# Performance work log

Measured on AMD Instinct MI355X. Metric: run time of the kernel, lower is better.

The kernel has to match this reference:

```python
import jax, jax.numpy as jnp
import numpy as np

B, T, D, H = 131072, 30, 10, 20
EPS = 1e-5


def setup_inputs() -> dict:
    key = jax.random.key(0)
    ks = jax.random.split(key, 8)
    rn = lambda k, s: (jax.random.normal(k, s, dtype=jnp.float32) * 0.1)
    return {
        "x": jax.random.normal(ks[0], (B, T, D), dtype=jnp.float32),
        "g0": jnp.ones((T, 2 * D), jnp.float32),
        "be0": jnp.zeros((T, 2 * D), jnp.float32),
        "W1": rn(ks[1], (T, H, 2 * D)),
        "b1": rn(ks[2], (T, H)),
        "g1": jnp.ones((T, H), jnp.float32),
        "be1": jnp.zeros((T, H), jnp.float32),
        "W2": rn(ks[3], (T, H, H)),
        "b2": rn(ks[4], (T, H)),
        "g2": jnp.ones((T, H), jnp.float32),
        "be2": jnp.zeros((T, H), jnp.float32),
        "W3": rn(ks[5], (T, D, H)),
        "b3": rn(ks[6], (T, D)),
    }


def _bn(x, g, b):
    # training-mode BatchNorm1d: batch stats, biased variance, eps=1e-5
    mu = x.mean(0)
    var = ((x - mu) ** 2).mean(0)
    return (x - mu) * jax.lax.rsqrt(var + EPS) * g + b


def _forward(x, g0, be0, W1, b1, g1, be1, W2, b2, g2, be2, W3, b3):
    xs = jnp.swapaxes(x, 0, 1)  # [T, B, D] time-major

    def step(prev, ps):
        xt, g0t, be0t, W1t, b1t, g1t, be1t, W2t, b2t, g2t, be2t, W3t, b3t = ps
        h = jnp.concatenate([xt, prev], axis=1)      # [B, 2D] recurrent concat
        h = _bn(h, g0t, be0t)
        h = jax.nn.relu(_bn(h @ W1t.T + b1t, g1t, be1t))  # [B, H]
        h = jax.nn.relu(_bn(h @ W2t.T + b2t, g2t, be2t))  # [B, H]
        out = h @ W3t.T + b3t                              # [B, D]
        return out, out

    init = jnp.zeros((x.shape[0], D), dtype=x.dtype)
    _, outs = jax.lax.scan(step, init, (xs, g0, be0, W1, b1, g1, be1, W2, b2, g2, be2, W3, b3))
    return jnp.swapaxes(outs, 0, 1)  # [B, T, D]


def reference(x, g0, be0, W1, b1, g1, be1, W2, b2, g2, be2, W3, b3):
    return _forward(x, g0, be0, W1, b1, g1, be1, W2, b2, g2, be2, W3, b3)
```

## Files before the change

kernel.cpp:

```cpp
#include <hip/hip_runtime.h>

static constexpr int   BATCH = 131072;
static constexpr int   TS    = 30;
static constexpr int   DD    = 10;
static constexpr int   HH    = 20;
static constexpr float EPSV  = 1e-5f;
static constexpr float INV_B = 1.0f / (float)BATCH;

static constexpr int NBLK = 256;
static constexpr int NTHR = 256;
static constexpr int RPT  = 2;
static constexpr int TT   = NBLK * NTHR;
static constexpr int NS   = 8;
static constexpr int GRPS = 8;
static constexpr int GSZ  = NBLK / GRPS;
static constexpr int NVA  = 230;
static constexpr int NVB  = 40;
static constexpr int STRA = NVA * NS;
static constexpr int STRB = NVB * NS;
static constexpr int CTRW = 160;
static constexpr int NPH  = 2 * TS + 1;

__device__ __forceinline__ int tri(int k, int l) {
    return k * (41 - k) / 2 + (l - k);
}

template <int CTRL>
__device__ __forceinline__ float dpp_add(float v) {
    int x = __builtin_amdgcn_update_dpp(0, __float_as_int(v), CTRL, 0xF, 0xF, true);
    return v + __int_as_float(x);
}

__device__ __forceinline__ float rowsum16(float v) {
    v = dpp_add<0x111>(v);
    v = dpp_add<0x112>(v);
    v = dpp_add<0x114>(v);
    v = dpp_add<0x118>(v);
    return v;
}

__device__ __forceinline__ float aloadf(const float* p) {
    return __hip_atomic_load(p, __ATOMIC_RELAXED, __HIP_MEMORY_SCOPE_AGENT);
}

__device__ __forceinline__ void gbar(unsigned* __restrict__ base, int tid, int grp8) {
    __syncthreads();
    if (tid == 0) {
        if (__hip_atomic_fetch_add(base + grp8 * 16, 1u, __ATOMIC_RELAXED,
                                   __HIP_MEMORY_SCOPE_AGENT) == (unsigned)(GSZ - 1))
            __hip_atomic_fetch_add(base + 128, 1u, __ATOMIC_RELAXED,
                                   __HIP_MEMORY_SCOPE_AGENT);
        while (__hip_atomic_load(base + 128, __ATOMIC_RELAXED,
                                 __HIP_MEMORY_SCOPE_AGENT) < (unsigned)GRPS)
            __builtin_amdgcn_s_sleep(1);
    }
    __syncthreads();
}

__global__ void __launch_bounds__(NTHR)
rnn_all(const float* __restrict__ x, float* __restrict__ outg,
        const float* __restrict__ W1, const float* __restrict__ W2,
        const float* __restrict__ W3, const float* __restrict__ b3,
        const float* __restrict__ g0, const float* __restrict__ be0,
        const float* __restrict__ g1, const float* __restrict__ be1,
        const float* __restrict__ g2, const float* __restrict__ be2,
        float* __restrict__ redA, float* __restrict__ redB,
        unsigned* __restrict__ ctr)
{
    __shared__ float lred[16 * NVA];
    __shared__ float sM[230], sMu[20], sCov[400], sU[400], sP[400];
    __shared__ float sW1[400], sW2[400], sW3[200], sB3[10];
    __shared__ float sA0[20], sC0[20], sA1[20], sC1[20], sA2[20], sC2[20];

    const int tid     = threadIdx.x;
    const int grp     = tid >> 4;
    const bool lane15 = (tid & 15) == 15;
    const int slot    = blockIdx.x & (NS - 1);
    const int grp8    = blockIdx.x & (GRPS - 1);
    const int gt      = blockIdx.x * NTHR + tid;

    float pv[RPT][DD];
#pragma unroll
    for (int r = 0; r < RPT; ++r)
#pragma unroll
        for (int d = 0; d < DD; ++d) pv[r][d] = 0.0f;

    float xv[RPT][DD];
#pragma unroll
    for (int r = 0; r < RPT; ++r) {
        const float2* px = reinterpret_cast<const float2*>(x + (size_t)(gt + r * TT) * TS * DD);
#pragma unroll
        for (int i = 0; i < 5; ++i) { float2 v = px[i]; xv[r][2 * i] = v.x; xv[r][2 * i + 1] = v.y; }
    }

#define H0A(i) ((i) < DD ? xv[0][i] : 0.0f)
#define H0B(i) ((i) < DD ? xv[1][i] : 0.0f)
    {
        int v = 0;
#pragma unroll
        for (int k = 0; k < 2 * DD; ++k) {
#pragma unroll
            for (int l = k; l < 2 * DD; ++l) {
                float p = fmaf(H0A(k), H0A(l), H0B(k) * H0B(l));
                float r = rowsum16(p);
                if (lane15) lred[grp * NVA + v] = r;
                ++v;
            }
        }
#pragma unroll
        for (int k = 0; k < 2 * DD; ++k) {
            float r = rowsum16(H0A(k) + H0B(k));
            if (lane15) lred[grp * NVA + 210 + k] = r;
        }
    }
#undef H0A
#undef H0B
    __syncthreads();
    if (tid < NVA) {
        float acc = 0.0f;
#pragma unroll
        for (int g = 0; g < 16; ++g) acc += lred[g * NVA + tid];
        atomicAdd(redA + tid * NS + slot, acc);
    }
    gbar(ctr + (size_t)(2 * TS) * CTRW, tid, grp8);

    for (int t = 0; t < TS; ++t) {
        for (int i = tid; i < 400; i += NTHR) { sW1[i] = W1[t * 400 + i]; sW2[i] = W2[t * 400 + i]; }
        if (tid < 200) sW3[tid] = W3[t * 200 + tid];
        if (tid >= 200 && tid < 210) sB3[tid - 200] = b3[t * DD + (tid - 200)];

        float xn[RPT][DD];
        if (t + 1 < TS) {
#pragma unroll
            for (int r = 0; r < RPT; ++r) {
                const float2* px = reinterpret_cast<const float2*>(x + (size_t)(gt + r * TT) * TS * DD + (t + 1) * DD);
#pragma unroll
                for (int i = 0; i < 5; ++i) { float2 v = px[i]; xn[r][2 * i] = v.x; xn[r][2 * i + 1] = v.y; }
            }
        }

        if (tid < NVA) {
            const float* p = redA + (size_t)t * STRA + tid * NS;
            float s = 0.0f;
#pragma unroll
            for (int i = 0; i < NS; ++i) s += aloadf(p + i);
            sM[tid] = s;
        }
        __syncthreads();

        if (tid < 20) {
            float mu  = sM[210 + tid] * INV_B;
            float var = fmaf(-mu, mu, sM[tri(tid, tid)] * INV_B);
            float a   = g0[t * 20 + tid] * rsqrtf(var + EPSV);
            sA0[tid] = a;
            sC0[tid] = fmaf(-mu, a, be0[t * 20 + tid]);
            sMu[tid] = mu;
        }
        __syncthreads();

        for (int i = tid; i < 400; i += NTHR) {
            int k = i / 20, l = i % 20;
            int a = k < l ? k : l, b = k < l ? l : k;
            sCov[i] = fmaf(-sMu[k], sMu[l], sM[tri(a, b)] * INV_B);
            sU[i]   = sW1[i] * sA0[l];
        }
        __syncthreads();

        for (int i = tid; i < 400; i += NTHR) {
            int j = i / 20, k = i % 20;
            float acc = 0.0f;
#pragma unroll
            for (int l = 0; l < 20; ++l)
                acc = fmaf(sCov[k * 20 + l], sU[j * 20 + l], acc);
            sP[i] = acc * sU[i];
        }
        __syncthreads();

        if (tid < 20) {
            float var1 = 0.0f, m1 = 0.0f;
#pragma unroll
            for (int k = 0; k < 20; ++k) {
                var1 += sP[tid * 20 + k];
                m1    = fmaf(sU[tid * 20 + k], sMu[k], m1);
                m1    = fmaf(sW1[tid * 20 + k], sC0[k], m1);
            }
            float a1 = g1[t * 20 + tid] * rsqrtf(var1 + EPSV);
            sA1[tid] = a1;
            sC1[tid] = fmaf(-m1, a1, be1[t * 20 + tid]);
        }
        __syncthreads();

        float y2[RPT][HH];
#pragma unroll
        for (int r = 0; r < RPT; ++r) {
            float hn[20];
#pragma unroll
            for (int k = 0; k < 10; ++k) hn[k]      = fmaf(xv[r][k], sA0[k],      sC0[k]);
#pragma unroll
            for (int k = 0; k < 10; ++k) hn[10 + k] = fmaf(pv[r][k], sA0[10 + k], sC0[10 + k]);

            float h1[20];
#pragma unroll
            for (int j = 0; j < 20; ++j) {
                float y = 0.0f;
#pragma unroll
                for (int k = 0; k < 20; ++k) y = fmaf(sW1[j * 20 + k], hn[k], y);
                h1[j] = fmaxf(fmaf(y, sA1[j], sC1[j]), 0.0f);
            }
#pragma unroll
            for (int j = 0; j < 20; ++j) {
                float y = 0.0f;
#pragma unroll
                for (int k = 0; k < 20; ++k) y = fmaf(sW2[j * 20 + k], h1[k], y);
                y2[r][j] = y;
            }
        }

#pragma unroll
        for (int j = 0; j < 20; ++j) {
            float r = rowsum16(y2[0][j] + y2[1][j]);
            if (lane15) lred[grp * NVA + j] = r;
        }
#pragma unroll
        for (int j = 0; j < 20; ++j) {
            float r = rowsum16(fmaf(y2[0][j], y2[0][j], y2[1][j] * y2[1][j]));
            if (lane15) lred[grp * NVA + 20 + j] = r;
        }
        __syncthreads();
        if (tid < NVB) {
            float acc = 0.0f;
#pragma unroll
            for (int g = 0; g < 16; ++g) acc += lred[g * NVA + tid];
            atomicAdd(redB + (size_t)t * STRB + tid * NS + slot, acc);
        }

        gbar(ctr + (size_t)(2 * t) * CTRW, tid, grp8);

        if (tid < NVB) {
            const float* p = redB + (size_t)t * STRB + tid * NS;
            float s = 0.0f;
#pragma unroll
            for (int i = 0; i < NS; ++i) s += aloadf(p + i);
            sM[tid] = s;
        }
        __syncthreads();
        if (tid < 20) {
            float m   = sM[tid] * INV_B;
            float var = fmaf(-m, m, sM[20 + tid] * INV_B);
            float a   = g2[t * 20 + tid] * rsqrtf(var + EPSV);
            sA2[tid] = a;
            sC2[tid] = fmaf(-m, a, be2[t * 20 + tid]);
        }
        __syncthreads();

        float ov[RPT][DD];
#pragma unroll
        for (int r = 0; r < RPT; ++r) {
            float h2[20];
#pragma unroll
            for (int j = 0; j < 20; ++j)
                h2[j] = fmaxf(fmaf(y2[r][j], sA2[j], sC2[j]), 0.0f);
#pragma unroll
            for (int d = 0; d < DD; ++d) {
                float a = sB3[d];
#pragma unroll
                for (int j = 0; j < 20; ++j)
                    a = fmaf(sW3[d * 20 + j], h2[j], a);
                ov[r][d] = a;
            }
            float2* po = reinterpret_cast<float2*>(outg + (size_t)(gt + r * TT) * TS * DD + t * DD);
#pragma unroll
            for (int i = 0; i < 5; ++i) po[i] = make_float2(ov[r][2 * i], ov[r][2 * i + 1]);
#pragma unroll
            for (int d = 0; d < DD; ++d) pv[r][d] = ov[r][d];
        }

        if (t + 1 < TS) {
#define H0A(i) ((i) < DD ? xn[0][i] : ov[0][(i) - DD])
#define H0B(i) ((i) < DD ? xn[1][i] : ov[1][(i) - DD])
            {
                int v = 0;
#pragma unroll
                for (int k = 0; k < 2 * DD; ++k) {
#pragma unroll
                    for (int l = k; l < 2 * DD; ++l) {
                        float p = fmaf(H0A(k), H0A(l), H0B(k) * H0B(l));
                        float r = rowsum16(p);
                        if (lane15) lred[grp * NVA + v] = r;
                        ++v;
                    }
                }
#pragma unroll
                for (int k = 0; k < 2 * DD; ++k) {
                    float r = rowsum16(H0A(k) + H0B(k));
                    if (lane15) lred[grp * NVA + 210 + k] = r;
                }
            }
#undef H0A
#undef H0B
            __syncthreads();
            if (tid < NVA) {
                float acc = 0.0f;
#pragma unroll
                for (int g = 0; g < 16; ++g) acc += lred[g * NVA + tid];
                atomicAdd(redA + (size_t)(t + 1) * STRA + tid * NS + slot, acc);
            }
            gbar(ctr + (size_t)(2 * t + 1) * CTRW, tid, grp8);

#pragma unroll
            for (int r = 0; r < RPT; ++r)
#pragma unroll
                for (int d = 0; d < DD; ++d) xv[r][d] = xn[r][d];
        }
    }
}

extern "C" void kernel_launch(void* const* d_in, const int* in_sizes, int n_in,
                              void* d_out, int out_size, void* d_ws, size_t ws_size,
                              hipStream_t stream) {
    const float* x   = (const float*)d_in[0];
    const float* g0  = (const float*)d_in[1];
    const float* be0 = (const float*)d_in[2];
    const float* W1  = (const float*)d_in[3];
    const float* b1  = (const float*)d_in[4];   (void)b1;
    const float* g1  = (const float*)d_in[5];
    const float* be1 = (const float*)d_in[6];
    const float* W2  = (const float*)d_in[7];
    const float* b2  = (const float*)d_in[8];   (void)b2;
    const float* g2  = (const float*)d_in[9];
    const float* be2 = (const float*)d_in[10];
    const float* W3  = (const float*)d_in[11];
    const float* b3  = (const float*)d_in[12];
    float* out = (float*)d_out;

    const size_t redA_f = (size_t)TS * STRA;
    const size_t redB_f = (size_t)TS * STRB;
    const size_t ctr_u  = (size_t)NPH * CTRW;
    float*    redA  = (float*)d_ws;
    float*    redB  = redA + redA_f;
    unsigned* ctr   = (unsigned*)(redB + redB_f);

    hipMemsetAsync(d_ws, 0, (redA_f + redB_f) * 4 + ctr_u * 4, stream);

    rnn_all<<<NBLK, NTHR, 0, stream>>>(x, out, W1, W2, W3, b3,
                                       g0, be0, g1, be1, g2, be2,
                                       redA, redB, ctr);
}
```

Before: 1.299 ms.

## Process one row per thread with 512 blocks and two blocks per CU

Switches from two batch rows per thread over 256 blocks to one row per thread over 512 blocks, with launch bounds requesting two resident blocks per CU. The grid barrier is widened to 16 groups with a larger counter stride. The aim is more resident waves and more latency hiding, in exchange for twice as many blocks taking part in each grid barrier and in the atomic reductions. It also loses the per-thread amortisation of the DPP row reductions across two rows.

```diff
diff --git a/kernel.cpp b/kernel.cpp
--- a/kernel.cpp
+++ b/kernel.cpp
@@ -7,18 +7,16 @@
 static constexpr float EPSV  = 1e-5f;
 static constexpr float INV_B = 1.0f / (float)BATCH;
 
-static constexpr int NBLK = 256;
+static constexpr int NBLK = 512;
 static constexpr int NTHR = 256;
-static constexpr int RPT  = 2;
-static constexpr int TT   = NBLK * NTHR;
 static constexpr int NS   = 8;
-static constexpr int GRPS = 8;
+static constexpr int GRPS = 16;
 static constexpr int GSZ  = NBLK / GRPS;
 static constexpr int NVA  = 230;
 static constexpr int NVB  = 40;
 static constexpr int STRA = NVA * NS;
 static constexpr int STRB = NVB * NS;
-static constexpr int CTRW = 160;
+static constexpr int CTRW = 288;
 static constexpr int NPH  = 2 * TS + 1;
 
 __device__ __forceinline__ int tri(int k, int l) {
@@ -43,21 +41,21 @@
     return __hip_atomic_load(p, __ATOMIC_RELAXED, __HIP_MEMORY_SCOPE_AGENT);
 }
 
-__device__ __forceinline__ void gbar(unsigned* __restrict__ base, int tid, int grp8) {
+__device__ __forceinline__ void gbar(unsigned* __restrict__ base, int tid, int grpN) {
     __syncthreads();
     if (tid == 0) {
-        if (__hip_atomic_fetch_add(base + grp8 * 16, 1u, __ATOMIC_RELAXED,
+        if (__hip_atomic_fetch_add(base + grpN * 16, 1u, __ATOMIC_RELAXED,
                                    __HIP_MEMORY_SCOPE_AGENT) == (unsigned)(GSZ - 1))
-            __hip_atomic_fetch_add(base + 128, 1u, __ATOMIC_RELAXED,
+            __hip_atomic_fetch_add(base + 256, 1u, __ATOMIC_RELAXED,
                                    __HIP_MEMORY_SCOPE_AGENT);
-        while (__hip_atomic_load(base + 128, __ATOMIC_RELAXED,
+        while (__hip_atomic_load(base + 256, __ATOMIC_RELAXED,
                                  __HIP_MEMORY_SCOPE_AGENT) < (unsigned)GRPS)
             __builtin_amdgcn_s_sleep(1);
     }
     __syncthreads();
 }
 
-__global__ void __launch_bounds__(NTHR)
+__global__ void __launch_bounds__(NTHR, 2)
 rnn_all(const float* __restrict__ x, float* __restrict__ outg,
         const float* __restrict__ W1, const float* __restrict__ W2,
         const float* __restrict__ W3, const float* __restrict__ b3,
@@ -76,45 +74,39 @@
     const int grp     = tid >> 4;
     const bool lane15 = (tid & 15) == 15;
     const int slot    = blockIdx.x & (NS - 1);
-    const int grp8    = blockIdx.x & (GRPS - 1);
-    const int gt      = blockIdx.x * NTHR + tid;
-
-    float pv[RPT][DD];
-#pragma unroll
-    for (int r = 0; r < RPT; ++r)
-#pragma unroll
-        for (int d = 0; d < DD; ++d) pv[r][d] = 0.0f;
-
-    float xv[RPT][DD];
-#pragma unroll
-    for (int r = 0; r < RPT; ++r) {
-        const float2* px = reinterpret_cast<const float2*>(x + (size_t)(gt + r * TT) * TS * DD);
-#pragma unroll
-        for (int i = 0; i < 5; ++i) { float2 v = px[i]; xv[r][2 * i] = v.x; xv[r][2 * i + 1] = v.y; }
-    }
-
-#define H0A(i) ((i) < DD ? xv[0][i] : 0.0f)
-#define H0B(i) ((i) < DD ? xv[1][i] : 0.0f)
+    const int grpN    = blockIdx.x & (GRPS - 1);
+    const int row     = blockIdx.x * NTHR + tid;
+
+    float pv[DD];
+#pragma unroll
+    for (int d = 0; d < DD; ++d) pv[d] = 0.0f;
+
+    float xv[DD];
+    {
+        const float2* px = reinterpret_cast<const float2*>(x + (size_t)row * TS * DD);
+#pragma unroll
+        for (int i = 0; i < 5; ++i) { float2 v = px[i]; xv[2 * i] = v.x; xv[2 * i + 1] = v.y; }
+    }
+
+#define H0(i) ((i) < DD ? xv[i] : 0.0f)
     {
         int v = 0;
 #pragma unroll
         for (int k = 0; k < 2 * DD; ++k) {
 #pragma unroll
             for (int l = k; l < 2 * DD; ++l) {
-                float p = fmaf(H0A(k), H0A(l), H0B(k) * H0B(l));
-                float r = rowsum16(p);
+                float r = rowsum16(H0(k) * H0(l));
                 if (lane15) lred[grp * NVA + v] = r;
                 ++v;
             }
         }
 #pragma unroll
         for (int k = 0; k < 2 * DD; ++k) {
-            float r = rowsum16(H0A(k) + H0B(k));
+            float r = rowsum16(H0(k));
             if (lane15) lred[grp * NVA + 210 + k] = r;
         }
     }
-#undef H0A
-#undef H0B
+#undef H0
     __syncthreads();
     if (tid < NVA) {
         float acc = 0.0f;
@@ -122,21 +114,18 @@
         for (int g = 0; g < 16; ++g) acc += lred[g * NVA + tid];
         atomicAdd(redA + tid * NS + slot, acc);
     }
-    gbar(ctr + (size_t)(2 * TS) * CTRW, tid, grp8);
+    gbar(ctr + (size_t)(2 * TS) * CTRW, tid, grpN);
 
     for (int t = 0; t < TS; ++t) {
         for (int i = tid; i < 400; i += NTHR) { sW1[i] = W1[t * 400 + i]; sW2[i] = W2[t * 400 + i]; }
         if (tid < 200) sW3[tid] = W3[t * 200 + tid];
         if (tid >= 200 && tid < 210) sB3[tid - 200] = b3[t * DD + (tid - 200)];
 
-        float xn[RPT][DD];
+        float xn[DD];
         if (t + 1 < TS) {
-#pragma unroll
-            for (int r = 0; r < RPT; ++r) {
-                const float2* px = reinterpret_cast<const float2*>(x + (size_t)(gt + r * TT) * TS * DD + (t + 1) * DD);
-#pragma unroll
-                for (int i = 0; i < 5; ++i) { float2 v = px[i]; xn[r][2 * i] = v.x; xn[r][2 * i + 1] = v.y; }
-            }
+            const float2* px = reinterpret_cast<const float2*>(x + (size_t)row * TS * DD + (t + 1) * DD);
+#pragma unroll
+            for (int i = 0; i < 5; ++i) { float2 v = px[i]; xn[2 * i] = v.x; xn[2 * i + 1] = v.y; }
         }
 
         if (tid < NVA) {
@@ -190,14 +179,13 @@
         }
         __syncthreads();
 
-        float y2[RPT][HH];
-#pragma unroll
-        for (int r = 0; r < RPT; ++r) {
+        float y2[HH];
+        {
             float hn[20];
 #pragma unroll
-            for (int k = 0; k < 10; ++k) hn[k]      = fmaf(xv[r][k], sA0[k],      sC0[k]);
-#pragma unroll
-            for (int k = 0; k < 10; ++k) hn[10 + k] = fmaf(pv[r][k], sA0[10 + k], sC0[10 + k]);
+            for (int k = 0; k < 10; ++k) hn[k]      = fmaf(xv[k], sA0[k],      sC0[k]);
+#pragma unroll
+            for (int k = 0; k < 10; ++k) hn[10 + k] = fmaf(pv[k], sA0[10 + k], sC0[10 + k]);
 
             float h1[20];
 #pragma unroll
@@ -212,18 +200,18 @@
                 float y = 0.0f;
 #pragma unroll
                 for (int k = 0; k < 20; ++k) y = fmaf(sW2[j * 20 + k], h1[k], y);
-                y2[r][j] = y;
+                y2[j] = y;
             }
         }
 
 #pragma unroll
         for (int j = 0; j < 20; ++j) {
-            float r = rowsum16(y2[0][j] + y2[1][j]);
+            float r = rowsum16(y2[j]);
             if (lane15) lred[grp * NVA + j] = r;
         }
 #pragma unroll
         for (int j = 0; j < 20; ++j) {
-            float r = rowsum16(fmaf(y2[0][j], y2[0][j], y2[1][j] * y2[1][j]));
+            float r = rowsum16(y2[j] * y2[j]);
             if (lane15) lred[grp * NVA + 20 + j] = r;
         }
         __syncthreads();
@@ -234,7 +222,7 @@
             atomicAdd(redB + (size_t)t * STRB + tid * NS + slot, acc);
         }
 
-        gbar(ctr + (size_t)(2 * t) * CTRW, tid, grp8);
+        gbar(ctr + (size_t)(2 * t) * CTRW, tid, grpN);
 
         if (tid < NVB) {
             const float* p = redB + (size_t)t * STRB + tid * NS;
@@ -253,51 +241,47 @@
         }
         __syncthreads();
 
-        float ov[RPT][DD];
-#pragma unroll
-        for (int r = 0; r < RPT; ++r) {
+        float ov[DD];
+        {
             float h2[20];
 #pragma unroll
             for (int j = 0; j < 20; ++j)
-                h2[j] = fmaxf(fmaf(y2[r][j], sA2[j], sC2[j]), 0.0f);
+                h2[j] = fmaxf(fmaf(y2[j], sA2[j], sC2[j]), 0.0f);
 #pragma unroll
             for (int d = 0; d < DD; ++d) {
                 float a = sB3[d];
 #pragma unroll
                 for (int j = 0; j < 20; ++j)
                     a = fmaf(sW3[d * 20 + j], h2[j], a);
-                ov[r][d] = a;
-            }
-            float2* po = reinterpret_cast<float2*>(outg + (size_t)(gt + r * TT) * TS * DD + t * DD);
-#pragma unroll
-            for (int i = 0; i < 5; ++i) po[i] = make_float2(ov[r][2 * i], ov[r][2 * i + 1]);
-#pragma unroll
-            for (int d = 0; d < DD; ++d) pv[r][d] = ov[r][d];
+                ov[d] = a;
+            }
+            float2* po = reinterpret_cast<float2*>(outg + (size_t)row * TS * DD + t * DD);
+#pragma unroll
+            for (int i = 0; i < 5; ++i) po[i] = make_float2(ov[2 * i], ov[2 * i + 1]);
+#pragma unroll
+            for (int d = 0; d < DD; ++d) pv[d] = ov[d];
         }
 
         if (t + 1 < TS) {
-#define H0A(i) ((i) < DD ? xn[0][i] : ov[0][(i) - DD])
-#define H0B(i) ((i) < DD ? xn[1][i] : ov[1][(i) - DD])
+#define H0(i) ((i) < DD ? xn[i] : ov[(i) - DD])
             {
                 int v = 0;
 #pragma unroll
                 for (int k = 0; k < 2 * DD; ++k) {
 #pragma unroll
                     for (int l = k; l < 2 * DD; ++l) {
-                        float p = fmaf(H0A(k), H0A(l), H0B(k) * H0B(l));
-                        float r = rowsum16(p);
+                        float r = rowsum16(H0(k) * H0(l));
                         if (lane15) lred[grp * NVA + v] = r;
                         ++v;
                     }
                 }
 #pragma unroll
                 for (int k = 0; k < 2 * DD; ++k) {
-                    float r = rowsum16(H0A(k) + H0B(k));
+                    float r = rowsum16(H0(k));
                     if (lane15) lred[grp * NVA + 210 + k] = r;
                 }
             }
-#undef H0A
-#undef H0B
+#undef H0
             __syncthreads();
             if (tid < NVA) {
                 float acc = 0.0f;
@@ -305,12 +289,10 @@
                 for (int g = 0; g < 16; ++g) acc += lred[g * NVA + tid];
                 atomicAdd(redA + (size_t)(t + 1) * STRA + tid * NS + slot, acc);
             }
-            gbar(ctr + (size_t)(2 * t + 1) * CTRW, tid, grp8);
-
-#pragma unroll
-            for (int r = 0; r < RPT; ++r)
-#pragma unroll
-                for (int d = 0; d < DD; ++d) xv[r][d] = xn[r][d];
+            gbar(ctr + (size_t)(2 * t + 1) * CTRW, tid, grpN);
+
+#pragma unroll
+            for (int d = 0; d < DD; ++d) xv[d] = xn[d];
         }
     }
 }
```

After: 3.671 ms. 2.82x slower.

## Precompute x-only covariance terms before barrier and widen barrier groups to 16

Applied to the files above, without the earlier changes.

The layer-0 BatchNorm statistics for the next step are split: the x-only second moments and sums (which depend only on the prefetched next input) are now reduced and atomically accumulated before the mid-step grid barrier, leaving only the x·prev cross terms and prev-only terms on the critical path after the output is known. The hierarchical grid barrier also uses 16 groups instead of 8, with the counter stride widened to fit. This shortens the serialized work between the last two barriers of each step, at the cost of an extra block-level sync and more atomics earlier in the step.

```diff
diff --git a/kernel.cpp b/kernel.cpp
--- a/kernel.cpp
+++ b/kernel.cpp
@@ -12,13 +12,13 @@
 static constexpr int RPT  = 2;
 static constexpr int TT   = NBLK * NTHR;
 static constexpr int NS   = 8;
-static constexpr int GRPS = 8;
+static constexpr int GRPS = 16;
 static constexpr int GSZ  = NBLK / GRPS;
 static constexpr int NVA  = 230;
 static constexpr int NVB  = 40;
 static constexpr int STRA = NVA * NS;
 static constexpr int STRB = NVB * NS;
-static constexpr int CTRW = 160;
+static constexpr int CTRW = 272;
 static constexpr int NPH  = 2 * TS + 1;
 
 __device__ __forceinline__ int tri(int k, int l) {
@@ -43,14 +43,14 @@
     return __hip_atomic_load(p, __ATOMIC_RELAXED, __HIP_MEMORY_SCOPE_AGENT);
 }
 
-__device__ __forceinline__ void gbar(unsigned* __restrict__ base, int tid, int grp8) {
+__device__ __forceinline__ void gbar(unsigned* __restrict__ base, int tid, int grpN) {
     __syncthreads();
     if (tid == 0) {
-        if (__hip_atomic_fetch_add(base + grp8 * 16, 1u, __ATOMIC_RELAXED,
+        if (__hip_atomic_fetch_add(base + grpN * 16, 1u, __ATOMIC_RELAXED,
                                    __HIP_MEMORY_SCOPE_AGENT) == (unsigned)(GSZ - 1))
-            __hip_atomic_fetch_add(base + 128, 1u, __ATOMIC_RELAXED,
+            __hip_atomic_fetch_add(base + 256, 1u, __ATOMIC_RELAXED,
                                    __HIP_MEMORY_SCOPE_AGENT);
-        while (__hip_atomic_load(base + 128, __ATOMIC_RELAXED,
+        while (__hip_atomic_load(base + 256, __ATOMIC_RELAXED,
                                  __HIP_MEMORY_SCOPE_AGENT) < (unsigned)GRPS)
             __builtin_amdgcn_s_sleep(1);
     }
@@ -76,7 +76,7 @@
     const int grp     = tid >> 4;
     const bool lane15 = (tid & 15) == 15;
     const int slot    = blockIdx.x & (NS - 1);
-    const int grp8    = blockIdx.x & (GRPS - 1);
+    const int grpN    = blockIdx.x & (GRPS - 1);
     const int gt      = blockIdx.x * NTHR + tid;
 
     float pv[RPT][DD];
@@ -122,7 +122,7 @@
         for (int g = 0; g < 16; ++g) acc += lred[g * NVA + tid];
         atomicAdd(redA + tid * NS + slot, acc);
     }
-    gbar(ctr + (size_t)(2 * TS) * CTRW, tid, grp8);
+    gbar(ctr + (size_t)(2 * TS) * CTRW, tid, grpN);
 
     for (int t = 0; t < TS; ++t) {
         for (int i = tid; i < 400; i += NTHR) { sW1[i] = W1[t * 400 + i]; sW2[i] = W2[t * 400 + i]; }
@@ -198,7 +198,6 @@
             for (int k = 0; k < 10; ++k) hn[k]      = fmaf(xv[r][k], sA0[k],      sC0[k]);
 #pragma unroll
             for (int k = 0; k < 10; ++k) hn[10 + k] = fmaf(pv[r][k], sA0[10 + k], sC0[10 + k]);
-
             float h1[20];
 #pragma unroll
             for (int j = 0; j < 20; ++j) {
@@ -214,6 +213,41 @@
                 for (int k = 0; k < 20; ++k) y = fmaf(sW2[j * 20 + k], h1[k], y);
                 y2[r][j] = y;
             }
+        }
+
+        if (t + 1 < TS) {
+            int c = 0;
+#pragma unroll
+            for (int k = 0; k < DD; ++k) {
+#pragma unroll
+                for (int l = k; l < DD; ++l) {
+                    float p = fmaf(xn[0][k], xn[0][l], xn[1][k] * xn[1][l]);
+                    float r = rowsum16(p);
+                    if (lane15) lred[grp * NVA + c] = r;
+                    ++c;
+                }
+            }
+#pragma unroll
+            for (int k = 0; k < DD; ++k) {
+                float r = rowsum16(xn[0][k] + xn[1][k]);
+                if (lane15) lred[grp * NVA + 55 + k] = r;
+            }
+            __syncthreads();
+            if (tid < 65) {
+                float acc = 0.0f;
+#pragma unroll
+                for (int g = 0; g < 16; ++g) acc += lred[g * NVA + tid];
+                int v;
+                if (tid < 55) {
+                    int c2 = tid, k = 0;
+                    while (c2 >= DD - k) { c2 -= DD - k; ++k; }
+                    v = tri(k, k + c2);
+                } else {
+                    v = 210 + (tid - 55);
+                }
+                atomicAdd(redA + (size_t)(t + 1) * STRA + v * NS + slot, acc);
+            }
+            __syncthreads();
         }
 
 #pragma unroll
@@ -234,7 +268,7 @@
             atomicAdd(redB + (size_t)t * STRB + tid * NS + slot, acc);
         }
 
-        gbar(ctr + (size_t)(2 * t) * CTRW, tid, grp8);
+        gbar(ctr + (size_t)(2 * t) * CTRW, tid, grpN);
 
         if (tid < NVB) {
             const float* p = redB + (size_t)t * STRB + tid * NS;
@@ -276,36 +310,52 @@
         }
 
         if (t + 1 < TS) {
-#define H0A(i) ((i) < DD ? xn[0][i] : ov[0][(i) - DD])
-#define H0B(i) ((i) < DD ? xn[1][i] : ov[1][(i) - DD])
             {
-                int v = 0;
-#pragma unroll
-                for (int k = 0; k < 2 * DD; ++k) {
-#pragma unroll
-                    for (int l = k; l < 2 * DD; ++l) {
-                        float p = fmaf(H0A(k), H0A(l), H0B(k) * H0B(l));
+                int c = 0;
+#pragma unroll
+                for (int k = 0; k < DD; ++k) {
+#pragma unroll
+                    for (int l = 0; l < DD; ++l) {
+                        float p = fmaf(xn[0][k], ov[0][l], xn[1][k] * ov[1][l]);
                         float r = rowsum16(p);
-                        if (lane15) lred[grp * NVA + v] = r;
-                        ++v;
+                        if (lane15) lred[grp * NVA + c] = r;
+                        ++c;
                     }
                 }
 #pragma unroll
-                for (int k = 0; k < 2 * DD; ++k) {
-                    float r = rowsum16(H0A(k) + H0B(k));
-                    if (lane15) lred[grp * NVA + 210 + k] = r;
-                }
-            }
-#undef H0A
-#undef H0B
+                for (int a = 0; a < DD; ++a) {
+#pragma unroll
+                    for (int b = a; b < DD; ++b) {
+                        float p = fmaf(ov[0][a], ov[0][b], ov[1][a] * ov[1][b]);
+                        float r = rowsum16(p);
+                        if (lane15) lred[grp * NVA + c] = r;
+                        ++c;
+                    }
+                }
+#pragma unroll
+                for (int d = 0; d < DD; ++d) {
+                    float r = rowsum16(ov[0][d] + ov[1][d]);
+                    if (lane15) lred[grp * NVA + 155 + d] = r;
+                }
+            }
             __syncthreads();
-            if (tid < NVA) {
+            if (tid < 165) {
                 float acc = 0.0f;
 #pragma unroll
                 for (int g = 0; g < 16; ++g) acc += lred[g * NVA + tid];
-                atomicAdd(redA + (size_t)(t + 1) * STRA + tid * NS + slot, acc);
-            }
-            gbar(ctr + (size_t)(2 * t + 1) * CTRW, tid, grp8);
+                int v;
+                if (tid < 100) {
+                    v = tri(tid / 10, 10 + tid % 10);
+                } else if (tid < 155) {
+                    int c2 = tid - 100, a = 0;
+                    while (c2 >= DD - a) { c2 -= DD - a; ++a; }
+                    v = tri(10 + a, 10 + a + c2);
+                } else {
+                    v = 220 + (tid - 155);
+                }
+                atomicAdd(redA + (size_t)(t + 1) * STRA + v * NS + slot, acc);
+            }
+            gbar(ctr + (size_t)(2 * t + 1) * CTRW, tid, grpN);
 
 #pragma unroll
             for (int r = 0; r < RPT; ++r)
```

Result: slower. 2.555 ms (+96.6%).
